# Kernel optimization log

Hardware: AMD Instinct MI355X
Metric: run time of the kernel (lower is better)

## Reference

```python
import jax, jax.numpy as jnp
import numpy as np

D = 1024
M = 16
H = D // M  # 64
EPS = 1e-05


def setup_inputs() -> dict:
    key = jax.random.key(0)
    ks = jax.random.split(key, 5)
    B, T = 4, 1024
    x = jax.random.normal(ks[0], (B, T, D), dtype=jnp.float32)
    norm_w = jnp.ones((D,), dtype=jnp.float32)
    s = 1.0 / np.sqrt(D)
    W_v = jax.random.uniform(ks[1], (D, D), dtype=jnp.float32, minval=-s, maxval=s)
    W_a = jax.random.uniform(ks[2], (H * M * (M + 1), D), dtype=jnp.float32, minval=-s, maxval=s)
    W_out = jax.random.uniform(ks[3], (D, D), dtype=jnp.float32, minval=-s, maxval=s)
    return {"x": x, "norm_w": norm_w, "W_v": W_v, "W_a": W_a, "W_out": W_out}


def _rmsnorm(x, w, eps=EPS):
    var = jnp.mean(jnp.square(x), axis=-1, keepdims=True)
    return x * jax.lax.rsqrt(var + eps) * w


def reference(x, norm_w, W_v, W_a, W_out):
    B, T, _ = x.shape
    h = _rmsnorm(x, norm_w)                              # [B,T,D]
    v = (h @ W_v.T).reshape(B, T, H, M)                  # [B,T,H,m]
    gate_logits = (h @ W_a.T).reshape(B, T, H, M, M + 1)
    gates = jax.nn.softmax(gate_logits, axis=-1)
    a0 = gates[..., 0]                                   # [B,T,H,m]
    A = gates[..., 1:]                                   # [B,T,H,m,m]

    # time-major for scan
    A_t = jnp.moveaxis(A, 1, 0)                          # [T,B,H,m,m]
    u_t = jnp.moveaxis(a0 * v, 1, 0)                     # [T,B,H,m]

    def step(state, inp):
        At, ut = inp
        new = jnp.einsum('bhij,bhj->bhi', At, state) + ut
        return new, new

    init = jnp.zeros((B, H, M), dtype=x.dtype)
    _, ys = jax.lax.scan(step, init, (A_t, u_t))         # ys: [T,B,H,m]
    h_out = jnp.moveaxis(ys, 0, 1).reshape(B, T, D)
    return x + h_out @ W_out.T
```

## Files before the change

kernel.cpp:

```cpp
#include <hip/hip_runtime.h>
#include <hip/hip_bf16.h>
#include <math.h>

#define B_DIM 4
#define T_DIM 1024
#define D_DIM 1024
#define M_DIM 16
#define H_DIM 64
#define NT    4096
#define NA    17408
#define EPSV  1e-5f
#define CL    16
#define NC    64

typedef __bf16 bf16_t;
typedef __bf16 bf16x4 __attribute__((ext_vector_type(4)));
typedef __bf16 bf16x8 __attribute__((ext_vector_type(8)));
typedef float  f32x4  __attribute__((ext_vector_type(4)));

#define PBAR() do { asm volatile("" ::: "memory"); __builtin_amdgcn_s_barrier(); asm volatile("" ::: "memory"); } while (0)

__global__ __launch_bounds__(256) void cvt_kernel(const float* __restrict__ in,
                                                  bf16_t* __restrict__ out, int n4) {
  int idx = blockIdx.x * blockDim.x + threadIdx.x;
  int stride = gridDim.x * blockDim.x;
  for (; idx < n4; idx += stride) {
    float4 v = reinterpret_cast<const float4*>(in)[idx];
    bf16x4 o;
    o[0] = (bf16_t)v.x; o[1] = (bf16_t)v.y; o[2] = (bf16_t)v.z; o[3] = (bf16_t)v.w;
    reinterpret_cast<bf16x4*>(out)[idx] = o;
  }
}

__global__ __launch_bounds__(256) void rmsnorm_kernel(const float* __restrict__ x,
                                                      const float* __restrict__ w,
                                                      bf16_t* __restrict__ h) {
  int row = blockIdx.x;
  int tid = threadIdx.x;
  const float4* xr = reinterpret_cast<const float4*>(x + (size_t)row * D_DIM);
  float4 xv = xr[tid];
  float ss = xv.x * xv.x + xv.y * xv.y + xv.z * xv.z + xv.w * xv.w;
#pragma unroll
  for (int m = 1; m < 64; m <<= 1) ss += __shfl_xor(ss, m, 64);
  __shared__ float red[4];
  int lane = tid & 63, wid = tid >> 6;
  if (lane == 0) red[wid] = ss;
  __syncthreads();
  float tot = red[0] + red[1] + red[2] + red[3];
  float scale = rsqrtf(tot * (1.0f / D_DIM) + EPSV);
  float4 wv = reinterpret_cast<const float4*>(w)[tid];
  bf16x4 o;
  o[0] = (bf16_t)(xv.x * scale * wv.x);
  o[1] = (bf16_t)(xv.y * scale * wv.y);
  o[2] = (bf16_t)(xv.z * scale * wv.z);
  o[3] = (bf16_t)(xv.w * scale * wv.w);
  reinterpret_cast<bf16x4*>(h)[(size_t)row * 256 + tid] = o;
}

template <int OUT_MODE>
__global__ __launch_bounds__(256) void gemm_nt_kernel(const bf16_t* __restrict__ A,
                                                      const bf16_t* __restrict__ Bw,
                                                      void* __restrict__ Cout,
                                                      const float* __restrict__ resid,
                                                      int Mdim, int Ndim, int K) {
  constexpr int BM = 128, BN = 128, BK = 32;
  __shared__ bf16_t As[BM * BK];
  __shared__ bf16_t Bs[BN * BK];

  int tid = threadIdx.x;
  int lane = tid & 63;
  int wid = tid >> 6;
  int wm = wid >> 1, wn = wid & 1;
  int bm = blockIdx.x * BM;
  int bn = blockIdx.y * BN;
  int l15 = lane & 15;
  int l4 = lane >> 4;

  f32x4 acc[4][4];
#pragma unroll
  for (int i = 0; i < 4; i++)
#pragma unroll
    for (int j = 0; j < 4; j++) acc[i][j] = (f32x4){0.f, 0.f, 0.f, 0.f};

  const bf16_t* Ag = A + (size_t)bm * K;
  const bf16_t* Bg = Bw + (size_t)bn * K;
  int srow_lane = lane >> 2;
  int scol = (lane & 3) * 8;

  for (int k0 = 0; k0 < K; k0 += BK) {
#pragma unroll
    for (int i = 0; i < 2; i++) {
      int rbase = wid * 32 + i * 16;
      int r = rbase + srow_lane;
      __builtin_amdgcn_global_load_lds(
          (const __attribute__((address_space(1))) void*)(Ag + (size_t)r * K + k0 + scol),
          (__attribute__((address_space(3))) void*)(As + rbase * BK), 16, 0, 0);
      __builtin_amdgcn_global_load_lds(
          (const __attribute__((address_space(1))) void*)(Bg + (size_t)r * K + k0 + scol),
          (__attribute__((address_space(3))) void*)(Bs + rbase * BK), 16, 0, 0);
    }
    __syncthreads();

    const bf16x8* Asv = reinterpret_cast<const bf16x8*>(As);
    const bf16x8* Bsv = reinterpret_cast<const bf16x8*>(Bs);
    bf16x8 af[4], bfr[4];
#pragma unroll
    for (int mf = 0; mf < 4; mf++)
      af[mf] = Asv[(wm * 64 + mf * 16 + l15) * 4 + l4];
#pragma unroll
    for (int nf = 0; nf < 4; nf++)
      bfr[nf] = Bsv[(wn * 64 + nf * 16 + l15) * 4 + l4];
#pragma unroll
    for (int mf = 0; mf < 4; mf++)
#pragma unroll
      for (int nf = 0; nf < 4; nf++)
        acc[mf][nf] = __builtin_amdgcn_mfma_f32_16x16x32_bf16(af[mf], bfr[nf], acc[mf][nf], 0, 0, 0);
    __syncthreads();
  }

#pragma unroll
  for (int mf = 0; mf < 4; mf++)
#pragma unroll
    for (int nf = 0; nf < 4; nf++)
#pragma unroll
      for (int i = 0; i < 4; i++) {
        int row = bm + wm * 64 + mf * 16 + l4 * 4 + i;
        int col = bn + wn * 64 + nf * 16 + l15;
        size_t idx = (size_t)row * Ndim + col;
        float val = acc[mf][nf][i];
        if (OUT_MODE == 0) {
          ((float*)Cout)[idx] = val;
        } else {
          ((float*)Cout)[idx] = val + resid[idx];
        }
      }
}

__global__ __launch_bounds__(512, 2) void gemm256_nt_kernel(const bf16_t* __restrict__ A,
                                                            const bf16_t* __restrict__ Bw,
                                                            bf16_t* __restrict__ C) {
  constexpr int K = 1024;
  constexpr int G = K / 64;
  __shared__ bf16_t As[2 * 16384];
  __shared__ bf16_t Bs[2 * 16384];

  const int tid = threadIdx.x;
  const int lane = tid & 63;
  const int w = tid >> 6;
  const int wm = w >> 2;
  const int wn = w & 3;
  const int l15 = lane & 15;
  const int l4 = lane >> 4;

  const int bm = blockIdx.x * 256;
  const int bn = blockIdx.y * 256;

  const bf16_t* Ag = A + (size_t)bm * K;
  const bf16_t* Bg = Bw + (size_t)bn * K;

  int growi[2], gcoli[2];
#pragma unroll
  for (int j = 0; j < 2; ++j) {
    int E = j * 4096 + tid * 8;
    int sub = E >> 9, e = E & 511;
    int rin = e >> 5, cs = e & 31;
    int cin = cs ^ ((rin & 8) ? 16 : 0);
    growi[j] = (sub >> 1) * 16 + rin;
    gcoli[j] = (sub & 1) * 32 + cin;
  }

  const int fbase = l15 * 32 + ((l4 * 8) ^ ((l15 & 8) ? 16 : 0));

  f32x4 acc[8][4];
#pragma unroll
  for (int i = 0; i < 8; i++)
#pragma unroll
    for (int j = 0; j < 4; j++) acc[i][j] = (f32x4){0.f, 0.f, 0.f, 0.f};

  bf16x8 ALo[8], AHi[8], B0r[4], B1r[4];

  auto stageHalf = [&](const bf16_t* Gp, bf16_t* Lp, int bufp, int half, int t2) {
#pragma unroll
    for (int j = 0; j < 2; ++j) {
      const bf16_t* src = Gp + (size_t)(half * 128 + growi[j]) * K + t2 * 64 + gcoli[j];
      __builtin_amdgcn_global_load_lds(
          (const __attribute__((address_space(1))) void*)src,
          (__attribute__((address_space(3))) void*)(Lp + bufp * 16384 + half * 8192 + j * 4096 + w * 512),
          16, 0, 0);
    }
  };

  auto rdA = [&](bf16x8* dst, int bufp, int rgrpBase) {
    const bf16_t* base = As + bufp * 16384;
#pragma unroll
    for (int mf = 0; mf < 4; ++mf)
#pragma unroll
      for (int kk = 0; kk < 2; ++kk)
        dst[mf * 2 + kk] = *reinterpret_cast<const bf16x8*>(base + ((rgrpBase + mf) * 2 + kk) * 512 + fbase);
  };
  auto rdB = [&](bf16x8* dst, int bufp, int nfBase) {
    const bf16_t* base = Bs + bufp * 16384;
#pragma unroll
    for (int nf = 0; nf < 2; ++nf)
#pragma unroll
      for (int kk = 0; kk < 2; ++kk)
        dst[nf * 2 + kk] = *reinterpret_cast<const bf16x8*>(base + ((wn * 4 + nfBase + nf) * 2 + kk) * 512 + fbase);
  };
  auto MM = [&](const bf16x8* Af, const bf16x8* Bf, int mfB, int nfB) {
    __builtin_amdgcn_s_setprio(1);
#pragma unroll
    for (int mf = 0; mf < 4; ++mf)
#pragma unroll
      for (int nf = 0; nf < 2; ++nf)
#pragma unroll
        for (int kk = 0; kk < 2; ++kk)
          acc[mfB + mf][nfB + nf] = __builtin_amdgcn_mfma_f32_16x16x32_bf16(
              Af[mf * 2 + kk], Bf[nf * 2 + kk], acc[mfB + mf][nfB + nf], 0, 0, 0);
    __builtin_amdgcn_s_setprio(0);
  };

  stageHalf(Bg, Bs, 0, 0, 0);
  stageHalf(Bg, Bs, 0, 1, 0);
  stageHalf(Ag, As, 0, 0, 0);
  stageHalf(Ag, As, 0, 1, 0);
  stageHalf(Ag, As, 1, 0, 1);
  stageHalf(Ag, As, 1, 1, 1);
  asm volatile("s_waitcnt vmcnt(0)" ::: "memory");
  PBAR();
  rdA(ALo, 0, wm * 8);

#pragma unroll 1
  for (int t = 0; t < G; ++t) {
    const int buf = t & 1;
    const int nbuf = buf ^ 1;

    rdB(B0r, buf, 0);
    if (t + 1 < G) stageHalf(Bg, Bs, nbuf, 0, t + 1);
    PBAR();
    MM(ALo, B0r, 0, 0);
    PBAR();

    rdB(B1r, buf, 2);
    rdA(AHi, buf, wm * 8 + 4);
    if (t + 1 < G) stageHalf(Bg, Bs, nbuf, 1, t + 1);
    PBAR();
    MM(ALo, B1r, 0, 2);
    if (t + 1 < G) {
      if (t + 2 < G) asm volatile("s_waitcnt vmcnt(4)" ::: "memory");
      else           asm volatile("s_waitcnt vmcnt(4)" ::: "memory");
    }
    PBAR();

    if (t + 1 < G) rdA(ALo, nbuf, wm * 8);
    if (t + 2 < G) stageHalf(Ag, As, buf, 0, t + 2);
    PBAR();
    MM(AHi, B0r, 4, 0);
    PBAR();

    if (t + 2 < G) stageHalf(Ag, As, buf, 1, t + 2);
    PBAR();
    MM(AHi, B1r, 4, 2);
    if (t + 2 < G)      asm volatile("s_waitcnt vmcnt(4)" ::: "memory");
    else if (t + 1 < G) asm volatile("s_waitcnt vmcnt(0)" ::: "memory");
    PBAR();
  }

#pragma unroll
  for (int mf = 0; mf < 8; ++mf)
#pragma unroll
    for (int nf = 0; nf < 4; ++nf)
#pragma unroll
      for (int i = 0; i < 4; ++i) {
        int row = bm + wm * 128 + mf * 16 + l4 * 4 + i;
        int col = bn + wn * 64 + nf * 16 + l15;
        C[(size_t)row * NA + col] = (bf16_t)acc[mf][nf][i];
      }
}

__device__ __forceinline__ void softmax17(const bf16_t* __restrict__ lp, float vval,
                                          f32x4& a0, f32x4& a1, f32x4& a2, f32x4& a3,
                                          float& u) {
  float e[17];
  float mx = -1e30f;
#pragma unroll
  for (int j = 0; j < 17; ++j) {
    e[j] = (float)lp[j];
    mx = fmaxf(mx, e[j]);
  }
  float s = 0.f;
#pragma unroll
  for (int j = 0; j < 17; ++j) {
    e[j] = __expf(e[j] - mx);
    s += e[j];
  }
  float inv = 1.0f / s;
  a0 = (f32x4){e[1] * inv, e[2] * inv, e[3] * inv, e[4] * inv};
  a1 = (f32x4){e[5] * inv, e[6] * inv, e[7] * inv, e[8] * inv};
  a2 = (f32x4){e[9] * inv, e[10] * inv, e[11] * inv, e[12] * inv};
  a3 = (f32x4){e[13] * inv, e[14] * inv, e[15] * inv, e[16] * inv};
  u = e[0] * inv * vval;
}

__global__ __launch_bounds__(256) void scanA_kernel(const bf16_t* __restrict__ lg,
                                                    const float* __restrict__ v,
                                                    float* __restrict__ sum) {
  int bc = blockIdx.x;
  int b = bc >> 6;
  int c = bc & 63;
  int g = threadIdx.x >> 4;
  int i = threadIdx.x & 15;
  int h = blockIdx.y * 16 + g;
  int chain = b * 64 + h;

  __shared__ float Arows[16][16][16];
  __shared__ float Us[16][16];

  f32x4 R0 = (f32x4){i == 0 ? 1.f : 0.f, i == 1 ? 1.f : 0.f, i == 2 ? 1.f : 0.f, i == 3 ? 1.f : 0.f};
  f32x4 R1 = (f32x4){i == 4 ? 1.f : 0.f, i == 5 ? 1.f : 0.f, i == 6 ? 1.f : 0.f, i == 7 ? 1.f : 0.f};
  f32x4 R2 = (f32x4){i == 8 ? 1.f : 0.f, i == 9 ? 1.f : 0.f, i == 10 ? 1.f : 0.f, i == 11 ? 1.f : 0.f};
  f32x4 R3 = (f32x4){i == 12 ? 1.f : 0.f, i == 13 ? 1.f : 0.f, i == 14 ? 1.f : 0.f, i == 15 ? 1.f : 0.f};
  float q = 0.f;

#pragma unroll 1
  for (int tau = CL - 1; tau >= 0; --tau) {
    int r = b * T_DIM + c * CL + tau;
    const bf16_t* lp = lg + (size_t)r * NA + h * 272 + i * 17;
    float vval = v[(size_t)r * D_DIM + h * 16 + i];
    f32x4 a0, a1, a2, a3;
    float uu;
    softmax17(lp, vval, a0, a1, a2, a3, uu);

    *reinterpret_cast<f32x4*>(&Arows[g][i][0]) = a0;
    *reinterpret_cast<f32x4*>(&Arows[g][i][4]) = a1;
    *reinterpret_cast<f32x4*>(&Arows[g][i][8]) = a2;
    *reinterpret_cast<f32x4*>(&Arows[g][i][12]) = a3;
    Us[g][i] = uu;
    asm volatile("s_waitcnt lgkmcnt(0)" ::: "memory");
    __builtin_amdgcn_sched_barrier(0);

    f32x4 u0 = *reinterpret_cast<const f32x4*>(&Us[g][0]);
    f32x4 u1 = *reinterpret_cast<const f32x4*>(&Us[g][4]);
    f32x4 u2 = *reinterpret_cast<const f32x4*>(&Us[g][8]);
    f32x4 u3 = *reinterpret_cast<const f32x4*>(&Us[g][12]);
    float qa = fmaf(R0[0], u0[0], fmaf(R0[1], u0[1], fmaf(R0[2], u0[2], R0[3] * u0[3])));
    float qb = fmaf(R1[0], u1[0], fmaf(R1[1], u1[1], fmaf(R1[2], u1[2], R1[3] * u1[3])));
    float qc = fmaf(R2[0], u2[0], fmaf(R2[1], u2[1], fmaf(R2[2], u2[2], R2[3] * u2[3])));
    float qd = fmaf(R3[0], u3[0], fmaf(R3[1], u3[1], fmaf(R3[2], u3[2], R3[3] * u3[3])));
    q += (qa + qb) + (qc + qd);

    f32x4 n0 = (f32x4){0.f, 0.f, 0.f, 0.f}, n1 = n0, n2 = n0, n3 = n0;
#pragma unroll
    for (int k = 0; k < 16; ++k) {
      float rk = (k < 4) ? R0[k & 3] : (k < 8) ? R1[k & 3] : (k < 12) ? R2[k & 3] : R3[k & 3];
      f32x4 b0 = *reinterpret_cast<const f32x4*>(&Arows[g][k][0]);
      f32x4 b1 = *reinterpret_cast<const f32x4*>(&Arows[g][k][4]);
      f32x4 b2 = *reinterpret_cast<const f32x4*>(&Arows[g][k][8]);
      f32x4 b3 = *reinterpret_cast<const f32x4*>(&Arows[g][k][12]);
#pragma unroll
      for (int e2 = 0; e2 < 4; ++e2) {
        n0[e2] = fmaf(rk, b0[e2], n0[e2]);
        n1[e2] = fmaf(rk, b1[e2], n1[e2]);
        n2[e2] = fmaf(rk, b2[e2], n2[e2]);
        n3[e2] = fmaf(rk, b3[e2], n3[e2]);
      }
    }
    R0 = n0; R1 = n1; R2 = n2; R3 = n3;
  }

  float* sp = sum + (size_t)(chain * NC + c) * 272;
  *reinterpret_cast<f32x4*>(&sp[i * 16 + 0]) = R0;
  *reinterpret_cast<f32x4*>(&sp[i * 16 + 4]) = R1;
  *reinterpret_cast<f32x4*>(&sp[i * 16 + 8]) = R2;
  *reinterpret_cast<f32x4*>(&sp[i * 16 + 12]) = R3;
  sp[256 + i] = q;
}

__global__ __launch_bounds__(64) void scanB_kernel(const float* __restrict__ sum,
                                                   float* __restrict__ sinit) {
  int chain = blockIdx.x;
  int lane = threadIdx.x;
  int i = lane & 15;

  __shared__ float seg[2][2176];

  const float* gbase = sum + (size_t)chain * NC * 272;

  auto load_seg = [&](int s, int buf) {
#pragma unroll
    for (int r = 0; r < 9; ++r) {
      int idx = r * 256 + lane * 4;
      if (idx < 2176) {
        __builtin_amdgcn_global_load_lds(
            (const __attribute__((address_space(1))) void*)(gbase + (size_t)s * 2176 + idx),
            (__attribute__((address_space(3))) void*)(&seg[buf][r * 256]), 16, 0, 0);
      }
    }
  };

  load_seg(0, 0);
  asm volatile("s_waitcnt vmcnt(0)" ::: "memory");
  __builtin_amdgcn_sched_barrier(0);

  f32x4 S0 = (f32x4){0.f, 0.f, 0.f, 0.f}, S1 = S0, S2 = S0, S3 = S0;
  float own = 0.f;

  for (int sg = 0; sg < 8; ++sg) {
    int buf = sg & 1;
    if (sg + 1 < 8) load_seg(sg + 1, buf ^ 1);
#pragma unroll 1
    for (int cc = 0; cc < 8; ++cc) {
      int c = sg * 8 + cc;
      const float* Pb = &seg[buf][cc * 272];
      if (lane < 16) sinit[(size_t)(chain * NC + c) * 16 + i] = own;

      f32x4 p0 = *reinterpret_cast<const f32x4*>(&Pb[i * 16 + 0]);
      f32x4 p1 = *reinterpret_cast<const f32x4*>(&Pb[i * 16 + 4]);
      f32x4 p2 = *reinterpret_cast<const f32x4*>(&Pb[i * 16 + 8]);
      f32x4 p3 = *reinterpret_cast<const f32x4*>(&Pb[i * 16 + 12]);
      float qq = Pb[256 + i];

      float pa = fmaf(p0[0], S0[0], fmaf(p0[1], S0[1], fmaf(p0[2], S0[2], p0[3] * S0[3])));
      float pb = fmaf(p1[0], S1[0], fmaf(p1[1], S1[1], fmaf(p1[2], S1[2], p1[3] * S1[3])));
      float pc = fmaf(p2[0], S2[0], fmaf(p2[1], S2[1], fmaf(p2[2], S2[2], p2[3] * S2[3])));
      float pd = fmaf(p3[0], S3[0], fmaf(p3[1], S3[1], fmaf(p3[2], S3[2], p3[3] * S3[3])));
      float p = (pa + pb) + (pc + pd) + qq;
      own = p;

#pragma unroll
      for (int j = 0; j < 4; ++j) {
        S0[j] = __shfl(p, j, 64);
        S1[j] = __shfl(p, 4 + j, 64);
        S2[j] = __shfl(p, 8 + j, 64);
        S3[j] = __shfl(p, 12 + j, 64);
      }
    }
    if (sg + 1 < 8) {
      asm volatile("s_waitcnt vmcnt(0)" ::: "memory");
      __builtin_amdgcn_sched_barrier(0);
    }
  }
}

__global__ __launch_bounds__(256) void scanC_kernel(const bf16_t* __restrict__ lg,
                                                    const float* __restrict__ v,
                                                    const float* __restrict__ sinit,
                                                    bf16_t* __restrict__ y) {
  int bc = blockIdx.x;
  int b = bc >> 6;
  int c = bc & 63;
  int g = threadIdx.x >> 4;
  int i = threadIdx.x & 15;
  int h = blockIdx.y * 16 + g;
  int chain = b * 64 + h;

  __shared__ float Sb[16][16];

  const float* ip = sinit + (size_t)(chain * NC + c) * 16;
  f32x4 S0 = *reinterpret_cast<const f32x4*>(&ip[0]);
  f32x4 S1 = *reinterpret_cast<const f32x4*>(&ip[4]);
  f32x4 S2 = *reinterpret_cast<const f32x4*>(&ip[8]);
  f32x4 S3 = *reinterpret_cast<const f32x4*>(&ip[12]);

#pragma unroll 1
  for (int t = 0; t < CL; ++t) {
    int r = b * T_DIM + c * CL + t;
    const bf16_t* lp = lg + (size_t)r * NA + h * 272 + i * 17;
    float vval = v[(size_t)r * D_DIM + h * 16 + i];
    f32x4 a0, a1, a2, a3;
    float uu;
    softmax17(lp, vval, a0, a1, a2, a3, uu);

    float pa = fmaf(a0[0], S0[0], fmaf(a0[1], S0[1], fmaf(a0[2], S0[2], a0[3] * S0[3])));
    float pb = fmaf(a1[0], S1[0], fmaf(a1[1], S1[1], fmaf(a1[2], S1[2], a1[3] * S1[3])));
    float pc = fmaf(a2[0], S2[0], fmaf(a2[1], S2[1], fmaf(a2[2], S2[2], a2[3] * S2[3])));
    float pd = fmaf(a3[0], S3[0], fmaf(a3[1], S3[1], fmaf(a3[2], S3[2], a3[3] * S3[3])));
    float p = (pa + pb) + (pc + pd) + uu;

    y[(size_t)r * D_DIM + h * 16 + i] = (bf16_t)p;

    Sb[g][i] = p;
    asm volatile("s_waitcnt lgkmcnt(0)" ::: "memory");
    __builtin_amdgcn_sched_barrier(0);
    S0 = *reinterpret_cast<const f32x4*>(&Sb[g][0]);
    S1 = *reinterpret_cast<const f32x4*>(&Sb[g][4]);
    S2 = *reinterpret_cast<const f32x4*>(&Sb[g][8]);
    S3 = *reinterpret_cast<const f32x4*>(&Sb[g][12]);
  }
}

extern "C" void kernel_launch(void* const* d_in, const int* in_sizes, int n_in,
                              void* d_out, int out_size, void* d_ws, size_t ws_size,
                              hipStream_t stream) {
  const float* x      = (const float*)d_in[0];
  const float* norm_w = (const float*)d_in[1];
  const float* W_v    = (const float*)d_in[2];
  const float* W_a    = (const float*)d_in[3];
  const float* W_out  = (const float*)d_in[4];

  char* ws = (char*)d_ws;
  size_t off = 0;
  auto alloc = [&](size_t bytes) {
    void* p = ws + off;
    off += (bytes + 255) & ~(size_t)255;
    return p;
  };
  bf16_t* wv_b = (bf16_t*)alloc((size_t)D_DIM * D_DIM * 2);
  bf16_t* wa_b = (bf16_t*)alloc((size_t)NA * D_DIM * 2);
  bf16_t* wo_b = (bf16_t*)alloc((size_t)D_DIM * D_DIM * 2);
  bf16_t* h_b  = (bf16_t*)alloc((size_t)NT * D_DIM * 2);
  float*  v_f  = (float*)alloc((size_t)NT * D_DIM * 4);
  bf16_t* lg_b = (bf16_t*)alloc((size_t)NT * NA * 2);
  bf16_t* y_b  = (bf16_t*)alloc((size_t)NT * D_DIM * 2);
  float*  sum_f   = (float*)alloc((size_t)256 * NC * 272 * 4);
  float*  sinit_f = (float*)alloc((size_t)256 * NC * 16 * 4);

  cvt_kernel<<<1024, 256, 0, stream>>>(W_v, wv_b, D_DIM * D_DIM / 4);
  cvt_kernel<<<1024, 256, 0, stream>>>(W_a, wa_b, NA * D_DIM / 4);
  cvt_kernel<<<1024, 256, 0, stream>>>(W_out, wo_b, D_DIM * D_DIM / 4);

  rmsnorm_kernel<<<NT, 256, 0, stream>>>(x, norm_w, h_b);

  gemm_nt_kernel<0><<<dim3(NT / 128, D_DIM / 128), 256, 0, stream>>>(
      h_b, wv_b, (void*)v_f, nullptr, NT, D_DIM, D_DIM);

  gemm256_nt_kernel<<<dim3(NT / 256, NA / 256), 512, 0, stream>>>(h_b, wa_b, lg_b);

  scanA_kernel<<<dim3(256, 4), 256, 0, stream>>>(lg_b, v_f, sum_f);
  scanB_kernel<<<256, 64, 0, stream>>>(sum_f, sinit_f);
  scanC_kernel<<<dim3(256, 4), 256, 0, stream>>>(lg_b, v_f, sinit_f, y_b);

  gemm_nt_kernel<2><<<dim3(NT / 128, D_DIM / 128), 256, 0, stream>>>(
      y_b, wo_b, d_out, x, NT, D_DIM, D_DIM);
}
```

Measured before the change: 366.0 us.

## Fuse W_v projection into big gate GEMM via concatenated weights

Concatenates W_a and W_v into one bf16 weight matrix so the V projection runs inside the 256x256 gate-logit GEMM, with blocks past column NA writing fp32 V output. The three weight-conversion launches are merged into one kernel. The AHi LDS reads are also split into two halves spread across the loop phases. This removes two launches and the smaller, less efficient 128-tile GEMM for V. The cost is a branch in the epilogue.

```diff
diff --git a/kernel.cpp b/kernel.cpp
--- a/kernel.cpp
+++ b/kernel.cpp
@@ -9,6 +9,7 @@
 #define H_DIM 64
 #define NT    4096
 #define NA    17408
+#define NCAT  18432
 #define EPSV  1e-5f
 #define CL    16
 #define NC    64
@@ -20,15 +21,25 @@
 
 #define PBAR() do { asm volatile("" ::: "memory"); __builtin_amdgcn_s_barrier(); asm volatile("" ::: "memory"); } while (0)
 
-__global__ __launch_bounds__(256) void cvt_kernel(const float* __restrict__ in,
-                                                  bf16_t* __restrict__ out, int n4) {
+__global__ __launch_bounds__(256) void cvt_all_kernel(const float* __restrict__ Wa,
+                                                      const float* __restrict__ Wv,
+                                                      const float* __restrict__ Wo,
+                                                      bf16_t* __restrict__ wcat,
+                                                      bf16_t* __restrict__ wo) {
+  constexpr int NA4 = NA * D_DIM / 4;
+  constexpr int NV4 = D_DIM * D_DIM / 4;
+  constexpr int total = NA4 + 2 * NV4;
   int idx = blockIdx.x * blockDim.x + threadIdx.x;
   int stride = gridDim.x * blockDim.x;
-  for (; idx < n4; idx += stride) {
-    float4 v = reinterpret_cast<const float4*>(in)[idx];
+  for (; idx < total; idx += stride) {
+    const float* src; bf16_t* dst; int j;
+    if (idx < NA4)            { src = Wa; dst = wcat; j = idx; }
+    else if (idx < NA4 + NV4) { src = Wv; dst = wcat + (size_t)NA * D_DIM; j = idx - NA4; }
+    else                      { src = Wo; dst = wo; j = idx - NA4 - NV4; }
+    float4 v = reinterpret_cast<const float4*>(src)[j];
     bf16x4 o;
     o[0] = (bf16_t)v.x; o[1] = (bf16_t)v.y; o[2] = (bf16_t)v.z; o[3] = (bf16_t)v.w;
-    reinterpret_cast<bf16x4*>(out)[idx] = o;
+    reinterpret_cast<bf16x4*>(dst)[j] = o;
   }
 }
 
@@ -57,12 +68,11 @@
   reinterpret_cast<bf16x4*>(h)[(size_t)row * 256 + tid] = o;
 }
 
-template <int OUT_MODE>
-__global__ __launch_bounds__(256) void gemm_nt_kernel(const bf16_t* __restrict__ A,
-                                                      const bf16_t* __restrict__ Bw,
-                                                      void* __restrict__ Cout,
-                                                      const float* __restrict__ resid,
-                                                      int Mdim, int Ndim, int K) {
+__global__ __launch_bounds__(256) void gemm_out_kernel(const bf16_t* __restrict__ A,
+                                                       const bf16_t* __restrict__ Bw,
+                                                       float* __restrict__ Cout,
+                                                       const float* __restrict__ resid,
+                                                       int Ndim, int K) {
   constexpr int BM = 128, BN = 128, BK = 32;
   __shared__ bf16_t As[BM * BK];
   __shared__ bf16_t Bs[BN * BK];
@@ -127,18 +137,14 @@
         int row = bm + wm * 64 + mf * 16 + l4 * 4 + i;
         int col = bn + wn * 64 + nf * 16 + l15;
         size_t idx = (size_t)row * Ndim + col;
-        float val = acc[mf][nf][i];
-        if (OUT_MODE == 0) {
-          ((float*)Cout)[idx] = val;
-        } else {
-          ((float*)Cout)[idx] = val + resid[idx];
-        }
+        Cout[idx] = acc[mf][nf][i] + resid[idx];
       }
 }
 
 __global__ __launch_bounds__(512, 2) void gemm256_nt_kernel(const bf16_t* __restrict__ A,
                                                             const bf16_t* __restrict__ Bw,
-                                                            bf16_t* __restrict__ C) {
+                                                            bf16_t* __restrict__ Clg,
+                                                            float* __restrict__ Cv) {
   constexpr int K = 1024;
   constexpr int G = K / 64;
   __shared__ bf16_t As[2 * 16384];
@@ -190,10 +196,18 @@
     }
   };
 
-  auto rdA = [&](bf16x8* dst, int bufp, int rgrpBase) {
+  auto rdA4 = [&](bf16x8* dst, int bufp, int rgrpBase) {
     const bf16_t* base = As + bufp * 16384;
 #pragma unroll
     for (int mf = 0; mf < 4; ++mf)
+#pragma unroll
+      for (int kk = 0; kk < 2; ++kk)
+        dst[mf * 2 + kk] = *reinterpret_cast<const bf16x8*>(base + ((rgrpBase + mf) * 2 + kk) * 512 + fbase);
+  };
+  auto rdA2 = [&](bf16x8* dst, int bufp, int rgrpBase) {
+    const bf16_t* base = As + bufp * 16384;
+#pragma unroll
+    for (int mf = 0; mf < 2; ++mf)
 #pragma unroll
       for (int kk = 0; kk < 2; ++kk)
         dst[mf * 2 + kk] = *reinterpret_cast<const bf16x8*>(base + ((rgrpBase + mf) * 2 + kk) * 512 + fbase);
@@ -227,7 +241,7 @@
   stageHalf(Ag, As, 1, 1, 1);
   asm volatile("s_waitcnt vmcnt(0)" ::: "memory");
   PBAR();
-  rdA(ALo, 0, wm * 8);
+  rdA4(ALo, 0, wm * 8);
 
 #pragma unroll 1
   for (int t = 0; t < G; ++t) {
@@ -235,23 +249,21 @@
     const int nbuf = buf ^ 1;
 
     rdB(B0r, buf, 0);
+    rdA2(AHi, buf, wm * 8 + 4);
     if (t + 1 < G) stageHalf(Bg, Bs, nbuf, 0, t + 1);
     PBAR();
     MM(ALo, B0r, 0, 0);
     PBAR();
 
     rdB(B1r, buf, 2);
-    rdA(AHi, buf, wm * 8 + 4);
+    rdA2(AHi + 4, buf, wm * 8 + 6);
     if (t + 1 < G) stageHalf(Bg, Bs, nbuf, 1, t + 1);
     PBAR();
     MM(ALo, B1r, 0, 2);
-    if (t + 1 < G) {
-      if (t + 2 < G) asm volatile("s_waitcnt vmcnt(4)" ::: "memory");
-      else           asm volatile("s_waitcnt vmcnt(4)" ::: "memory");
-    }
-    PBAR();
-
-    if (t + 1 < G) rdA(ALo, nbuf, wm * 8);
+    if (t + 1 < G) asm volatile("s_waitcnt vmcnt(4)" ::: "memory");
+    PBAR();
+
+    if (t + 1 < G) rdA4(ALo, nbuf, wm * 8);
     if (t + 2 < G) stageHalf(Ag, As, buf, 0, t + 2);
     PBAR();
     MM(AHi, B0r, 4, 0);
@@ -265,16 +277,30 @@
     PBAR();
   }
 
-#pragma unroll
-  for (int mf = 0; mf < 8; ++mf)
-#pragma unroll
-    for (int nf = 0; nf < 4; ++nf)
-#pragma unroll
-      for (int i = 0; i < 4; ++i) {
-        int row = bm + wm * 128 + mf * 16 + l4 * 4 + i;
-        int col = bn + wn * 64 + nf * 16 + l15;
-        C[(size_t)row * NA + col] = (bf16_t)acc[mf][nf][i];
-      }
+  if (blockIdx.y < 68) {
+#pragma unroll
+    for (int mf = 0; mf < 8; ++mf)
+#pragma unroll
+      for (int nf = 0; nf < 4; ++nf)
+#pragma unroll
+        for (int i = 0; i < 4; ++i) {
+          int row = bm + wm * 128 + mf * 16 + l4 * 4 + i;
+          int col = bn + wn * 64 + nf * 16 + l15;
+          Clg[(size_t)row * NA + col] = (bf16_t)acc[mf][nf][i];
+        }
+  } else {
+    int cb = bn - NA;
+#pragma unroll
+    for (int mf = 0; mf < 8; ++mf)
+#pragma unroll
+      for (int nf = 0; nf < 4; ++nf)
+#pragma unroll
+        for (int i = 0; i < 4; ++i) {
+          int row = bm + wm * 128 + mf * 16 + l4 * 4 + i;
+          int col = cb + wn * 64 + nf * 16 + l15;
+          Cv[(size_t)row * D_DIM + col] = acc[mf][nf][i];
+        }
+  }
 }
 
 __device__ __forceinline__ void softmax17(const bf16_t* __restrict__ lp, float vval,
@@ -504,8 +530,7 @@
     off += (bytes + 255) & ~(size_t)255;
     return p;
   };
-  bf16_t* wv_b = (bf16_t*)alloc((size_t)D_DIM * D_DIM * 2);
-  bf16_t* wa_b = (bf16_t*)alloc((size_t)NA * D_DIM * 2);
+  bf16_t* wcat = (bf16_t*)alloc((size_t)NCAT * D_DIM * 2);
   bf16_t* wo_b = (bf16_t*)alloc((size_t)D_DIM * D_DIM * 2);
   bf16_t* h_b  = (bf16_t*)alloc((size_t)NT * D_DIM * 2);
   float*  v_f  = (float*)alloc((size_t)NT * D_DIM * 4);
@@ -514,21 +539,16 @@
   float*  sum_f   = (float*)alloc((size_t)256 * NC * 272 * 4);
   float*  sinit_f = (float*)alloc((size_t)256 * NC * 16 * 4);
 
-  cvt_kernel<<<1024, 256, 0, stream>>>(W_v, wv_b, D_DIM * D_DIM / 4);
-  cvt_kernel<<<1024, 256, 0, stream>>>(W_a, wa_b, NA * D_DIM / 4);
-  cvt_kernel<<<1024, 256, 0, stream>>>(W_out, wo_b, D_DIM * D_DIM / 4);
+  cvt_all_kernel<<<2048, 256, 0, stream>>>(W_a, W_v, W_out, wcat, wo_b);
 
   rmsnorm_kernel<<<NT, 256, 0, stream>>>(x, norm_w, h_b);
 
-  gemm_nt_kernel<0><<<dim3(NT / 128, D_DIM / 128), 256, 0, stream>>>(
-      h_b, wv_b, (void*)v_f, nullptr, NT, D_DIM, D_DIM);
-
-  gemm256_nt_kernel<<<dim3(NT / 256, NA / 256), 512, 0, stream>>>(h_b, wa_b, lg_b);
+  gemm256_nt_kernel<<<dim3(NT / 256, NCAT / 256), 512, 0, stream>>>(h_b, wcat, lg_b, v_f);
 
   scanA_kernel<<<dim3(256, 4), 256, 0, stream>>>(lg_b, v_f, sum_f);
   scanB_kernel<<<256, 64, 0, stream>>>(sum_f, sinit_f);
   scanC_kernel<<<dim3(256, 4), 256, 0, stream>>>(lg_b, v_f, sinit_f, y_b);
 
-  gemm_nt_kernel<2><<<dim3(NT / 128, D_DIM / 128), 256, 0, stream>>>(
-      y_b, wo_b, d_out, x, NT, D_DIM, D_DIM);
-}
+  gemm_out_kernel<<<dim3(NT / 128, D_DIM / 128), 256, 0, stream>>>(
+      y_b, wo_b, (float*)d_out, x, D_DIM, D_DIM);
+}
```

After: 334.6 us. 8.6% less time.
